# Optimization experiments

Hardware: AMD Instinct MI355X
Metric: run time of the kernel (lower is better)

The kernel has to match this reference:

```python
import jax, jax.numpy as jnp
import numpy as np

N = 100_000      # nodes
E = 3_200_000    # edges (avg degree 32)
G = 1_000        # graphs (100 nodes each)
F_IN, H1, H2 = 3, 64, 128
MD, NC = 32, 10


def setup_inputs() -> dict:
    key = jax.random.key(0)
    ks = jax.random.split(key, 10)
    x = jax.random.normal(ks[0], (N, F_IN), dtype=jnp.float32)
    edge_index = jax.random.randint(ks[1], (2, E), 0, N, dtype=jnp.int64)
    batch = (jnp.arange(N) // (N // G)).astype(jnp.int32)  # sorted segment ids, all graphs non-empty
    moment_vecs = jax.random.normal(ks[2], (G, MD), dtype=jnp.float32)
    W1 = jax.random.normal(ks[3], (F_IN, H1), dtype=jnp.float32) * (1.0 / np.sqrt(F_IN))
    b1 = jnp.zeros((H1,), dtype=jnp.float32)
    W2 = jax.random.normal(ks[4], (H1, H2), dtype=jnp.float32) * (1.0 / np.sqrt(H1))
    b2 = jnp.zeros((H2,), dtype=jnp.float32)
    Wc1 = jax.random.normal(ks[5], (H2 + MD, H1), dtype=jnp.float32) * (1.0 / np.sqrt(H2 + MD))
    bc1 = jnp.zeros((H1,), dtype=jnp.float32)
    Wc2 = jax.random.normal(ks[6], (H1, NC), dtype=jnp.float32) * (1.0 / np.sqrt(H1))
    bc2 = jnp.zeros((NC,), dtype=jnp.float32)
    return dict(x=x, edge_index=edge_index, batch=batch, moment_vecs=moment_vecs,
                W1=W1, b1=b1, W2=W2, b2=b2, Wc1=Wc1, bc1=bc1, Wc2=Wc2, bc2=bc2)


def gcn_conv(x, row, col, norm, W, b, num_nodes):
    # PyG GCNConv: h = x @ W; out[col] += norm * h[row]; out += b
    h = x @ W
    msg = h[row] * norm[:, None]                      # [E+N, out_dim] gather
    out = jax.ops.segment_sum(msg, col, num_segments=num_nodes)
    return out + b


def reference(x, edge_index, batch, moment_vecs, W1, b1, W2, b2, Wc1, bc1, Wc2, bc2):
    n = x.shape[0]
    loop = jnp.arange(n, dtype=edge_index.dtype)
    row = jnp.concatenate([edge_index[0], loop])      # self-loops appended
    col = jnp.concatenate([edge_index[1], loop])
    deg = jax.ops.segment_sum(jnp.ones_like(col, dtype=x.dtype), col, num_segments=n)
    dinv = jnp.where(deg > 0, jax.lax.rsqrt(deg), 0.0)
    norm = dinv[row] * dinv[col]                      # D^{-1/2} (A+I) D^{-1/2}

    h = jax.nn.relu(gcn_conv(x, row, col, norm, W1, b1, n))
    h = jax.nn.relu(gcn_conv(h, row, col, norm, W2, b2, n))

    # global_mean_pool over batch segments
    counts = jax.ops.segment_sum(jnp.ones((n,), dtype=h.dtype), batch, num_segments=G)
    pooled = jax.ops.segment_sum(h, batch, num_segments=G) / jnp.maximum(counts, 1.0)[:, None]

    # graph_ids == arange(G) -> identity gather of moment_vecs
    z = jnp.concatenate([pooled, moment_vecs], axis=1)
    z = jax.nn.relu(z @ Wc1 + bc1)
    return z @ Wc2 + bc2
```

## Files before the change

### kernel.cpp

```cpp
#include <hip/hip_runtime.h>
#include <hip/hip_fp16.h>

#define NNODES 100000
#define NEDGES 3200000
#define NGRAPH 1000
#define NPG    100
#define MDIM   32
#define NCDIM  10

#define CAP     48
#define OVF_CAP 4096

#define NPART   8
#define PSIZE   12500
#define FCHUNK  6250
#define FBLKS   (NEDGES / FCHUNK)

#define W_S2    0
#define W_CNT   4800064
#define W_DINV  4900064
#define W_XD4   5000064
#define W_A4    5400064
#define W_G1H   5800064
#define W_OVF   9000064
#define WS_FLOATS 9008257

__global__ __launch_bounds__(256) void k_fillbkt(const int* __restrict__ ei,
                                                 int* __restrict__ cnt,
                                                 int* __restrict__ slot2,
                                                 int* __restrict__ ovf) {
    int part  = blockIdx.x & (NPART - 1);
    int chunk = blockIdx.x >> 3;
    int base  = chunk * FCHUNK;
    int end   = base + FCHUNK;
    int clo   = part * PSIZE;
    int chi   = clo + PSIZE;
    for (int e = base + threadIdx.x; e < end; e += 256) {
        int c = ei[NEDGES + e];
        if (c >= clo && c < chi) {
            int r = ei[e];
            int idx = atomicAdd(&cnt[c], 1);
            if (idx < CAP) {
                slot2[c * CAP + idx] = r;
            } else {
                int o = atomicAdd(&ovf[0], 1);
                if (o < OVF_CAP) { ovf[1 + 2 * o] = r; ovf[2 + 2 * o] = c; }
            }
        }
    }
}

__global__ __launch_bounds__(256) void k_prep(const int* __restrict__ cnt,
                                              const float* __restrict__ x,
                                              float* __restrict__ dinv,
                                              float4* __restrict__ xd4) {
    int i = blockIdx.x * blockDim.x + threadIdx.x;
    if (i >= NNODES) return;
    float di = rsqrtf((float)cnt[i] + 1.0f);
    dinv[i] = di;
    xd4[i] = make_float4(x[3 * i], x[3 * i + 1], x[3 * i + 2], di);
}

__global__ void k_a(const int* __restrict__ cnt, const int* __restrict__ slot2,
                    const float4* __restrict__ xd4, float4* __restrict__ a4) {
    int i = blockIdx.x * blockDim.x + threadIdx.x;
    if (i >= NNODES) return;
    int d = min(cnt[i], CAP);
    int s = i * CAP;
    int d8 = d & ~7;
    float ax = 0.f, ay = 0.f, az = 0.f;
    for (int k = 0; k < d8; k += 8) {
        float4 xr[8];
        #pragma unroll
        for (int j = 0; j < 8; ++j) xr[j] = xd4[slot2[s + k + j]];
        #pragma unroll
        for (int j = 0; j < 8; ++j) {
            ax += xr[j].w * xr[j].x; ay += xr[j].w * xr[j].y; az += xr[j].w * xr[j].z;
        }
    }
    if (d8 < d) {
        float4 xr[8];
        #pragma unroll
        for (int j = 0; j < 8; ++j) {
            int idx = slot2[s + d8 + j];
            xr[j] = xd4[(d8 + j < d) ? idx : 0];
        }
        #pragma unroll
        for (int j = 0; j < 8; ++j) {
            float u = (d8 + j < d) ? xr[j].w : 0.f;
            ax += u * xr[j].x; ay += u * xr[j].y; az += u * xr[j].z;
        }
    }
    float4 xi = xd4[i];
    float di = xi.w;
    a4[i] = make_float4(di * (ax + di * xi.x),
                        di * (ay + di * xi.y),
                        di * (az + di * xi.z), di);
}

__global__ void k_ovfA(const int* __restrict__ ovf, const float4* __restrict__ xd4,
                       const float* __restrict__ dinv, float* __restrict__ a4f) {
    int n = min(ovf[0], OVF_CAP);
    for (int k = threadIdx.x; k < n; k += 256) {
        int r = ovf[1 + 2 * k];
        int c = ovf[2 + 2 * k];
        float4 xr = xd4[r];
        float s = dinv[c] * xr.w;
        atomicAdd(&a4f[c * 4 + 0], s * xr.x);
        atomicAdd(&a4f[c * 4 + 1], s * xr.y);
        atomicAdd(&a4f[c * 4 + 2], s * xr.z);
    }
}

__global__ __launch_bounds__(256) void k_g1(const float4* __restrict__ a4,
                                            const float* __restrict__ W1,
                                            const float* __restrict__ b1,
                                            unsigned int* __restrict__ g1h) {
    int t = blockIdx.x * blockDim.x + threadIdx.x;
    int i = t >> 5, j = t & 31;
    if (i >= NNODES) return;
    float4 ai = a4[i];
    int f0 = 2 * j, f1 = f0 + 1;
    float h0 = fmaxf(ai.x * W1[f0] + ai.y * W1[64 + f0] + ai.z * W1[128 + f0] + b1[f0], 0.f);
    float h1 = fmaxf(ai.x * W1[f1] + ai.y * W1[64 + f1] + ai.z * W1[128 + f1] + b1[f1], 0.f);
    __half2 hv = __floats2half2_rn(ai.w * h0, ai.w * h1);
    g1h[t] = *(unsigned int*)&hv;
}

__global__ __launch_bounds__(512, 8) void k_fusedA(
    const int* __restrict__ cnt, const int* __restrict__ slot2,
    const int* __restrict__ ovf,
    const unsigned int* __restrict__ g1h, const float* __restrict__ dinv,
    const float* __restrict__ mv,
    const float* __restrict__ W2, const float* __restrict__ b2,
    const float* __restrict__ Wc1, const float* __restrict__ bc1,
    const float* __restrict__ Wc2, const float* __restrict__ bc2,
    float* __restrict__ out)
{
    __shared__ float aggh[NPG * 66];
    __shared__ float pools[8 * 128];
    __shared__ float zbuf[160];
    __shared__ float zz[64];

    int g = blockIdx.x;
    int t = threadIdx.x;
    int wb = t >> 6;
    int lane = t & 63;
    int h = lane >> 5;
    int j = lane & 31;
    int nn    = (wb < 4) ? 13 : 12;
    int rbase = (wb < 4) ? wb * 13 : 52 + (wb - 4) * 12;

    for (int i = 0; i < nn; ++i) {
        int n = rbase + i;
        int node = g * NPG + n;
        int s = node * CAP;
        int d = min(cnt[node], CAP);
        int d16 = d & ~15;
        float acc0 = 0.f, acc1 = 0.f;
        for (int k0 = 0; k0 < d16; k0 += 16) {
            int rr[8];
            #pragma unroll
            for (int jj = 0; jj < 8; ++jj)
                rr[jj] = slot2[s + k0 + 2 * jj + h];
            unsigned int pre[8];
            #pragma unroll
            for (int jj = 0; jj < 8; ++jj)
                pre[jj] = g1h[rr[jj] * 32 + j];
            #pragma unroll
            for (int jj = 0; jj < 8; ++jj) {
                float2 f = __half22float2(*(__half2*)&pre[jj]);
                acc0 += f.x;
                acc1 += f.y;
            }
        }
        if (d16 < d) {
            int rr[8];
            #pragma unroll
            for (int jj = 0; jj < 8; ++jj) {
                int pos = d16 + 2 * jj + h;
                int v = slot2[s + pos];
                rr[jj] = (pos < d) ? v : 0;
            }
            #pragma unroll
            for (int jj = 0; jj < 8; ++jj) {
                unsigned int v = g1h[rr[jj] * 32 + j];
                float2 f = __half22float2(*(__half2*)&v);
                bool ok = (d16 + 2 * jj + h) < d;
                acc0 += ok ? f.x : 0.f;
                acc1 += ok ? f.y : 0.f;
            }
        }
        acc0 += __shfl_xor(acc0, 32);
        acc1 += __shfl_xor(acc1, 32);
        if (h == 0) {
            unsigned int sv = g1h[node * 32 + j];
            float2 sf = __half22float2(*(__half2*)&sv);
            float dc = dinv[node];
            *(float2*)&aggh[n * 66 + 2 * j] =
                make_float2(dc * (acc0 + sf.x), dc * (acc1 + sf.y));
        }
    }
    {
        int novf = min(ovf[0], OVF_CAP);
        int glo = g * NPG;
        for (int k = 0; k < novf; ++k) {
            int r = ovf[1 + 2 * k];
            int c = ovf[2 + 2 * k];
            int n = c - glo;
            if (n >= rbase && n < rbase + nn && h == 0) {
                unsigned int v = g1h[r * 32 + j];
                float2 f = __half22float2(*(__half2*)&v);
                float dc = dinv[c];
                aggh[n * 66 + 2 * j]     += dc * f.x;
                aggh[n * 66 + 2 * j + 1] += dc * f.y;
            }
        }
    }

    float2 b2v = *(const float2*)&b2[2 * lane];
    float pool0 = 0.f, pool1 = 0.f;
    if (wb < 4) {
        float acc0[13], acc1[13];
        #pragma unroll
        for (int i = 0; i < 13; ++i) { acc0[i] = 0.f; acc1[i] = 0.f; }
        float2 wv0 = *(const float2*)&W2[2 * lane];
        float2 wv1 = *(const float2*)&W2[128 + 2 * lane];
        for (int f = 0; f < 64; ++f) {
            float2 wnx = (f + 2 < 64) ? *(const float2*)&W2[(f + 2) * 128 + 2 * lane] : wv0;
            #pragma unroll
            for (int i = 0; i < 13; ++i) {
                float rv = aggh[(rbase + i) * 66 + f];
                acc0[i] += rv * wv0.x;
                acc1[i] += rv * wv0.y;
            }
            wv0 = wv1; wv1 = wnx;
        }
        #pragma unroll
        for (int i = 0; i < 13; ++i) {
            pool0 += fmaxf(acc0[i] + b2v.x, 0.f);
            pool1 += fmaxf(acc1[i] + b2v.y, 0.f);
        }
    } else {
        float acc0[12], acc1[12];
        #pragma unroll
        for (int i = 0; i < 12; ++i) { acc0[i] = 0.f; acc1[i] = 0.f; }
        float2 wv0 = *(const float2*)&W2[2 * lane];
        float2 wv1 = *(const float2*)&W2[128 + 2 * lane];
        for (int f = 0; f < 64; ++f) {
            float2 wnx = (f + 2 < 64) ? *(const float2*)&W2[(f + 2) * 128 + 2 * lane] : wv0;
            #pragma unroll
            for (int i = 0; i < 12; ++i) {
                float rv = aggh[(rbase + i) * 66 + f];
                acc0[i] += rv * wv0.x;
                acc1[i] += rv * wv0.y;
            }
            wv0 = wv1; wv1 = wnx;
        }
        #pragma unroll
        for (int i = 0; i < 12; ++i) {
            pool0 += fmaxf(acc0[i] + b2v.x, 0.f);
            pool1 += fmaxf(acc1[i] + b2v.y, 0.f);
        }
    }

    pools[wb * 128 + 2 * lane]     = pool0;
    pools[wb * 128 + 2 * lane + 1] = pool1;
    __syncthreads();
    if (t < 128) {
        float z = 0.f;
        #pragma unroll
        for (int w = 0; w < 8; ++w) z += pools[w * 128 + t];
        zbuf[t] = z * (1.0f / NPG);
    }
    if (t < MDIM) zbuf[128 + t] = mv[g * MDIM + t];
    __syncthreads();
    if (t < 64) {
        float v = bc1[t];
        for (int k = 0; k < 160; ++k) v += zbuf[k] * Wc1[k * 64 + t];
        zz[t] = fmaxf(v, 0.f);
    }
    __syncthreads();
    if (t < NCDIM) {
        float o = bc2[t];
        #pragma unroll
        for (int k = 0; k < 64; ++k) o += zz[k] * Wc2[k * NCDIM + t];
        out[g * NCDIM + t] = o;
    }
}

extern "C" void kernel_launch(void* const* d_in, const int* in_sizes, int n_in,
                              void* d_out, int out_size, void* d_ws, size_t ws_size,
                              hipStream_t stream) {
    const float* x   = (const float*)d_in[0];
    const int*   ei  = (const int*)d_in[1];
    const float* mv  = (const float*)d_in[3];
    const float* W1  = (const float*)d_in[4];
    const float* b1  = (const float*)d_in[5];
    const float* W2  = (const float*)d_in[6];
    const float* b2  = (const float*)d_in[7];
    const float* Wc1 = (const float*)d_in[8];
    const float* bc1 = (const float*)d_in[9];
    const float* Wc2 = (const float*)d_in[10];
    const float* bc2 = (const float*)d_in[11];
    float* out = (float*)d_out;
    float* ws  = (float*)d_ws;

    if (ws_size < (size_t)WS_FLOATS * sizeof(float)) return;

    int*          slot2  = (int*)(ws + W_S2);
    int*          cnt    = (int*)(ws + W_CNT);
    float*        dinv   = ws + W_DINV;
    float4*       xd4    = (float4*)(ws + W_XD4);
    float4*       a4     = (float4*)(ws + W_A4);
    unsigned int* g1h    = (unsigned int*)(ws + W_G1H);
    int*          ovf    = (int*)(ws + W_OVF);

    hipMemsetAsync(cnt, 0, (size_t)NNODES * sizeof(int), stream);
    hipMemsetAsync(ovf, 0, sizeof(int), stream);

    k_fillbkt<<<FBLKS * NPART, 256, 0, stream>>>(ei, cnt, slot2, ovf);
    k_prep   <<<(NNODES + 255) / 256, 256, 0, stream>>>(cnt, x, dinv, xd4);
    k_a      <<<(NNODES + 255) / 256, 256, 0, stream>>>(cnt, slot2, xd4, a4);
    k_ovfA   <<<1, 256, 0, stream>>>(ovf, xd4, dinv, (float*)a4);
    k_g1     <<<(NNODES * 32) / 256, 256, 0, stream>>>(a4, W1, b1, g1h);
    k_fusedA <<<NGRAPH, 512, 0, stream>>>(cnt, slot2, ovf, g1h, dinv, mv,
                                          W2, b2, Wc1, bc1, Wc2, bc2, out);
}
```

Before: 342.8 us.

## Replace filtered edge bucketing with two-pass partition then scatter

The old fill kernel read every edge eight times, once per destination partition, keeping only edges in its range. The new code first bins edges by partition in shared memory and writes packed (row, local col) words to per-partition staging buffers, aliased over the g1h region. A second kernel scatters each partition's edges into per-node slots, so the edge list is read once and slot atomics stay localized per partition. The cost is an extra kernel launch, an extra staging write and read, and reliance on SCAP being large enough for partition skew.

After: 358.2 us. +4.5%, slower.

```diff
diff --git a/kernel.cpp b/kernel.cpp
--- a/kernel.cpp
+++ b/kernel.cpp
@@ -13,8 +13,10 @@
 
 #define NPART   8
 #define PSIZE   12500
-#define FCHUNK  6250
-#define FBLKS   (NEDGES / FCHUNK)
+#define SCAP    420000
+#define BIN_CAP 768
+#define PCHUNK  4096
+#define PBLKS   ((NEDGES + PCHUNK - 1) / PCHUNK)
 
 #define W_S2    0
 #define W_CNT   4800064
@@ -22,30 +24,73 @@
 #define W_XD4   5000064
 #define W_A4    5400064
 #define W_G1H   5800064
-#define W_OVF   9000064
-#define WS_FLOATS 9008257
-
-__global__ __launch_bounds__(256) void k_fillbkt(const int* __restrict__ ei,
-                                                 int* __restrict__ cnt,
-                                                 int* __restrict__ slot2,
-                                                 int* __restrict__ ovf) {
-    int part  = blockIdx.x & (NPART - 1);
-    int chunk = blockIdx.x >> 3;
-    int base  = chunk * FCHUNK;
-    int end   = base + FCHUNK;
-    int clo   = part * PSIZE;
-    int chi   = clo + PSIZE;
-    for (int e = base + threadIdx.x; e < end; e += 256) {
-        int c = ei[NEDGES + e];
-        if (c >= clo && c < chi) {
+#define W_OVF   9160064
+#define W_GCUR  9168260
+#define WS_FLOATS 9168300
+
+__global__ __launch_bounds__(256) void k_part(const int* __restrict__ ei,
+                                              int* __restrict__ stg,
+                                              int* __restrict__ gcur) {
+    __shared__ int bin[NPART][BIN_CAP];
+    __shared__ int bcnt[NPART];
+    __shared__ int bbase[NPART];
+    int base = blockIdx.x * PCHUNK;
+    int t = threadIdx.x;
+    if (t < NPART) bcnt[t] = 0;
+    __syncthreads();
+    #pragma unroll
+    for (int k = 0; k < PCHUNK / 256; ++k) {
+        int e = base + k * 256 + t;
+        if (e < NEDGES) {
+            int c = ei[NEDGES + e];
             int r = ei[e];
-            int idx = atomicAdd(&cnt[c], 1);
-            if (idx < CAP) {
-                slot2[c * CAP + idx] = r;
+            int p = c / PSIZE;
+            int st = r | ((c - p * PSIZE) << 17);
+            int idx = atomicAdd(&bcnt[p], 1);
+            if (idx < BIN_CAP) {
+                bin[p][idx] = st;
             } else {
-                int o = atomicAdd(&ovf[0], 1);
-                if (o < OVF_CAP) { ovf[1 + 2 * o] = r; ovf[2 + 2 * o] = c; }
-            }
+                int o = atomicAdd(&gcur[p], 1);
+                if (o < SCAP) stg[p * SCAP + o] = st;
+            }
+        }
+    }
+    __syncthreads();
+    if (t < NPART) {
+        int n = min(bcnt[t], BIN_CAP);
+        bbase[t] = atomicAdd(&gcur[t], n);
+    }
+    __syncthreads();
+    for (int p = 0; p < NPART; ++p) {
+        int n = min(bcnt[p], BIN_CAP);
+        int bb = bbase[p];
+        for (int i = t; i < n; i += 256) {
+            int o = bb + i;
+            if (o < SCAP) stg[p * SCAP + o] = bin[p][i];
+        }
+    }
+}
+
+__global__ __launch_bounds__(256) void k_scat(const int* __restrict__ stg,
+                                              const int* __restrict__ gcur,
+                                              int* __restrict__ cnt,
+                                              int* __restrict__ slot2,
+                                              int* __restrict__ ovf) {
+    int p  = blockIdx.x & (NPART - 1);
+    int wi = blockIdx.x >> 3;
+    int nb = gridDim.x >> 3;
+    int m = min(gcur[p], SCAP);
+    int clo = p * PSIZE;
+    for (int i = wi * 256 + threadIdx.x; i < m; i += nb * 256) {
+        int st = stg[p * SCAP + i];
+        int r = st & 0x1FFFF;
+        int c = clo + (st >> 17);
+        int idx = atomicAdd(&cnt[c], 1);
+        if (idx < CAP) {
+            slot2[c * CAP + idx] = r;
+        } else {
+            int o = atomicAdd(&ovf[0], 1);
+            if (o < OVF_CAP) { ovf[1 + 2 * o] = r; ovf[2 + 2 * o] = c; }
         }
     }
 }
@@ -313,13 +358,17 @@
     float*        dinv   = ws + W_DINV;
     float4*       xd4    = (float4*)(ws + W_XD4);
     float4*       a4     = (float4*)(ws + W_A4);
+    int*          stg    = (int*)(ws + W_G1H);
     unsigned int* g1h    = (unsigned int*)(ws + W_G1H);
     int*          ovf    = (int*)(ws + W_OVF);
+    int*          gcur   = (int*)(ws + W_GCUR);
 
     hipMemsetAsync(cnt, 0, (size_t)NNODES * sizeof(int), stream);
     hipMemsetAsync(ovf, 0, sizeof(int), stream);
-
-    k_fillbkt<<<FBLKS * NPART, 256, 0, stream>>>(ei, cnt, slot2, ovf);
+    hipMemsetAsync(gcur, 0, NPART * sizeof(int), stream);
+
+    k_part   <<<PBLKS, 256, 0, stream>>>(ei, stg, gcur);
+    k_scat   <<<64 * NPART, 256, 0, stream>>>(stg, gcur, cnt, slot2, ovf);
     k_prep   <<<(NNODES + 255) / 256, 256, 0, stream>>>(cnt, x, dinv, xd4);
     k_a      <<<(NNODES + 255) / 256, 256, 0, stream>>>(cnt, slot2, xd4, a4);
     k_ovfA   <<<1, 256, 0, stream>>>(ovf, xd4, dinv, (float*)a4);
```

## Split fp16 layer-1 features into four quarter planes for cache-local gathers

Applied to the files above, without the earlier changes.

The layer-1 half-precision features are written as four separate planes of 16 features each, and the fused kernel gathers one plane at a time. Each lane handles a different edge and loads 8 bytes, and the partial sums are combined with a cross-lane shuffle reduction. The aim is to shrink the gather working set per pass (about 3.2 MB per plane) so it fits in cache and is reused across edges. The cost is four passes over the edge lists and overflow entries, more shuffle reductions, and each gather touching only 32-byte segments. The shared-memory row pitch changes to 68 so the stores can be aligned float4 writes.

Result: slower. 776.2 us (+126.4%).

```diff
diff --git a/kernel.cpp b/kernel.cpp
--- a/kernel.cpp
+++ b/kernel.cpp
@@ -15,6 +15,8 @@
 #define PSIZE   12500
 #define FCHUNK  6250
 #define FBLKS   (NEDGES / FCHUNK)
+
+#define QSTRIDE 800000
 
 #define W_S2    0
 #define W_CNT   4800064
@@ -119,12 +121,13 @@
     int t = blockIdx.x * blockDim.x + threadIdx.x;
     int i = t >> 5, j = t & 31;
     if (i >= NNODES) return;
+    int q = j >> 3, l = j & 7;
     float4 ai = a4[i];
-    int f0 = 2 * j, f1 = f0 + 1;
+    int f0 = 16 * q + 2 * l, f1 = f0 + 1;
     float h0 = fmaxf(ai.x * W1[f0] + ai.y * W1[64 + f0] + ai.z * W1[128 + f0] + b1[f0], 0.f);
     float h1 = fmaxf(ai.x * W1[f1] + ai.y * W1[64 + f1] + ai.z * W1[128 + f1] + b1[f1], 0.f);
     __half2 hv = __floats2half2_rn(ai.w * h0, ai.w * h1);
-    g1h[t] = *(unsigned int*)&hv;
+    g1h[q * QSTRIDE + i * 8 + l] = *(unsigned int*)&hv;
 }
 
 __global__ __launch_bounds__(512, 8) void k_fusedA(
@@ -137,7 +140,7 @@
     const float* __restrict__ Wc2, const float* __restrict__ bc2,
     float* __restrict__ out)
 {
-    __shared__ float aggh[NPG * 66];
+    __shared__ float aggh[NPG * 68];
     __shared__ float pools[8 * 128];
     __shared__ float zbuf[160];
     __shared__ float zz[64];
@@ -146,74 +149,72 @@
     int t = threadIdx.x;
     int wb = t >> 6;
     int lane = t & 63;
-    int h = lane >> 5;
-    int j = lane & 31;
+    int es = lane >> 2;
+    int fq = lane & 3;
     int nn    = (wb < 4) ? 13 : 12;
     int rbase = (wb < 4) ? wb * 13 : 52 + (wb - 4) * 12;
 
-    for (int i = 0; i < nn; ++i) {
-        int n = rbase + i;
-        int node = g * NPG + n;
-        int s = node * CAP;
-        int d = min(cnt[node], CAP);
-        int d16 = d & ~15;
-        float acc0 = 0.f, acc1 = 0.f;
-        for (int k0 = 0; k0 < d16; k0 += 16) {
-            int rr[8];
+    for (int q = 0; q < 4; ++q) {
+        const unsigned int* gq = g1h + q * QSTRIDE;
+        for (int i = 0; i < nn; ++i) {
+            int n = rbase + i;
+            int node = g * NPG + n;
+            int s = node * CAP;
+            int d = min(cnt[node], CAP);
+            int d16 = d & ~15;
+            uint2 sv = *(const uint2*)&gq[node * 8 + 2 * fq];
+            float dc = dinv[node];
+            float acc0 = 0.f, acc1 = 0.f, acc2 = 0.f, acc3 = 0.f;
+            int rr = slot2[s + es];
+            for (int k0 = 0; k0 < d16; k0 += 16) {
+                uint2 pre = *(const uint2*)&gq[rr * 8 + 2 * fq];
+                int rrn = slot2[s + k0 + 16 + es];
+                float2 fA = __half22float2(*(__half2*)&pre.x);
+                float2 fB = __half22float2(*(__half2*)&pre.y);
+                acc0 += fA.x; acc1 += fA.y; acc2 += fB.x; acc3 += fB.y;
+                rr = rrn;
+            }
+            if (d16 < d) {
+                int pos = d16 + es;
+                bool ok = pos < d;
+                int rrt = ok ? rr : 0;
+                uint2 v = *(const uint2*)&gq[rrt * 8 + 2 * fq];
+                float2 fA = __half22float2(*(__half2*)&v.x);
+                float2 fB = __half22float2(*(__half2*)&v.y);
+                acc0 += ok ? fA.x : 0.f; acc1 += ok ? fA.y : 0.f;
+                acc2 += ok ? fB.x : 0.f; acc3 += ok ? fB.y : 0.f;
+            }
             #pragma unroll
-            for (int jj = 0; jj < 8; ++jj)
-                rr[jj] = slot2[s + k0 + 2 * jj + h];
-            unsigned int pre[8];
-            #pragma unroll
-            for (int jj = 0; jj < 8; ++jj)
-                pre[jj] = g1h[rr[jj] * 32 + j];
-            #pragma unroll
-            for (int jj = 0; jj < 8; ++jj) {
-                float2 f = __half22float2(*(__half2*)&pre[jj]);
-                acc0 += f.x;
-                acc1 += f.y;
-            }
-        }
-        if (d16 < d) {
-            int rr[8];
-            #pragma unroll
-            for (int jj = 0; jj < 8; ++jj) {
-                int pos = d16 + 2 * jj + h;
-                int v = slot2[s + pos];
-                rr[jj] = (pos < d) ? v : 0;
-            }
-            #pragma unroll
-            for (int jj = 0; jj < 8; ++jj) {
-                unsigned int v = g1h[rr[jj] * 32 + j];
-                float2 f = __half22float2(*(__half2*)&v);
-                bool ok = (d16 + 2 * jj + h) < d;
-                acc0 += ok ? f.x : 0.f;
-                acc1 += ok ? f.y : 0.f;
-            }
-        }
-        acc0 += __shfl_xor(acc0, 32);
-        acc1 += __shfl_xor(acc1, 32);
-        if (h == 0) {
-            unsigned int sv = g1h[node * 32 + j];
-            float2 sf = __half22float2(*(__half2*)&sv);
-            float dc = dinv[node];
-            *(float2*)&aggh[n * 66 + 2 * j] =
-                make_float2(dc * (acc0 + sf.x), dc * (acc1 + sf.y));
-        }
-    }
-    {
+            for (int st = 4; st < 64; st <<= 1) {
+                acc0 += __shfl_xor(acc0, st);
+                acc1 += __shfl_xor(acc1, st);
+                acc2 += __shfl_xor(acc2, st);
+                acc3 += __shfl_xor(acc3, st);
+            }
+            if (lane < 4) {
+                float2 sA = __half22float2(*(__half2*)&sv.x);
+                float2 sB = __half22float2(*(__half2*)&sv.y);
+                *(float4*)&aggh[n * 68 + 16 * q + 4 * fq] =
+                    make_float4(dc * (acc0 + sA.x), dc * (acc1 + sA.y),
+                                dc * (acc2 + sB.x), dc * (acc3 + sB.y));
+            }
+        }
         int novf = min(ovf[0], OVF_CAP);
         int glo = g * NPG;
         for (int k = 0; k < novf; ++k) {
             int r = ovf[1 + 2 * k];
             int c = ovf[2 + 2 * k];
             int n = c - glo;
-            if (n >= rbase && n < rbase + nn && h == 0) {
-                unsigned int v = g1h[r * 32 + j];
-                float2 f = __half22float2(*(__half2*)&v);
+            if (n >= rbase && n < rbase + nn && lane < 4) {
+                uint2 v = *(const uint2*)&gq[r * 8 + 2 * fq];
+                float2 fA = __half22float2(*(__half2*)&v.x);
+                float2 fB = __half22float2(*(__half2*)&v.y);
                 float dc = dinv[c];
-                aggh[n * 66 + 2 * j]     += dc * f.x;
-                aggh[n * 66 + 2 * j + 1] += dc * f.y;
+                int cb = n * 68 + 16 * q + 4 * fq;
+                aggh[cb + 0] += dc * fA.x;
+                aggh[cb + 1] += dc * fA.y;
+                aggh[cb + 2] += dc * fB.x;
+                aggh[cb + 3] += dc * fB.y;
             }
         }
     }
@@ -230,7 +231,7 @@
             float2 wnx = (f + 2 < 64) ? *(const float2*)&W2[(f + 2) * 128 + 2 * lane] : wv0;
             #pragma unroll
             for (int i = 0; i < 13; ++i) {
-                float rv = aggh[(rbase + i) * 66 + f];
+                float rv = aggh[(rbase + i) * 68 + f];
                 acc0[i] += rv * wv0.x;
                 acc1[i] += rv * wv0.y;
             }
@@ -251,7 +252,7 @@
             float2 wnx = (f + 2 < 64) ? *(const float2*)&W2[(f + 2) * 128 + 2 * lane] : wv0;
             #pragma unroll
             for (int i = 0; i < 12; ++i) {
-                float rv = aggh[(rbase + i) * 66 + f];
+                float rv = aggh[(rbase + i) * 68 + f];
                 acc0[i] += rv * wv0.x;
                 acc1[i] += rv * wv0.y;
             }
```
